# Kernel tuning notes

Measured on AMD Instinct MI355X. Metric: run time of the kernel, lower is better.

The kernel has to match this reference:

```python
import jax, jax.numpy as jnp
import numpy as np

NUM_HEADS = 8
KEY_DIM = 512      # total projected dim across heads
VALUE_DIM = 512
EMBED_DIM = 512


def setup_inputs() -> dict:
    key = jax.random.key(0)
    ks = jax.random.split(key, 12)
    B, S, E = 8, 1024, EMBED_DIM
    sc_in = 1.0 / np.sqrt(E)
    sc_o = 1.0 / np.sqrt(KEY_DIM)
    return {
        "queries": jax.random.normal(ks[0], (B, S, E), jnp.float32),
        "keys": jax.random.normal(ks[1], (B, S, E), jnp.float32),
        "values": jax.random.normal(ks[2], (B, S, E), jnp.float32),
        "Wq": jax.random.normal(ks[3], (E, KEY_DIM), jnp.float32) * sc_in,
        "bq": jnp.zeros((KEY_DIM,), jnp.float32),
        "Wk": jax.random.normal(ks[4], (E, KEY_DIM), jnp.float32) * sc_in,
        "bk": jnp.zeros((KEY_DIM,), jnp.float32),
        "Wv": jax.random.normal(ks[5], (E, VALUE_DIM), jnp.float32) * sc_in,
        "bv": jnp.zeros((VALUE_DIM,), jnp.float32),
        "Wo": jax.random.normal(ks[6], (KEY_DIM, EMBED_DIM), jnp.float32) * sc_o,
        "bo": jnp.zeros((EMBED_DIM,), jnp.float32),
    }


def _split_heads(x):
    # [B, S, key_dim] -> [B, H, S, key_dim//H]
    B, S, D = x.shape
    return x.reshape(B, S, NUM_HEADS, D // NUM_HEADS).transpose(0, 2, 1, 3)


def reference(queries, keys, values, Wq, bq, Wk, bk, Wv, bv, Wo, bo):
    q = _split_heads(queries @ Wq + bq)   # [B,H,S,dh]
    k = _split_heads(keys @ Wk + bk)
    v = _split_heads(values @ Wv + bv)
    # NOTE: original scales by sqrt(full key_dim), not per-head dim
    scores = jnp.einsum("bhqd,bhkd->bhqk", q, k) / jnp.sqrt(
        jnp.asarray(KEY_DIM, jnp.float32))
    weights = jax.nn.softmax(scores, axis=-1)
    o = jnp.einsum("bhqk,bhkd->bhqd", weights, v)  # [B,H,S,dh]
    B, H, S, dh = o.shape
    o = o.transpose(0, 2, 1, 3).reshape(B, S, H * dh)  # merge heads -> key_dim
    return o @ Wo + bo
```

## Files before the change

### kernel.cpp

```cpp
#include <hip/hip_runtime.h>


typedef __bf16 bf16x8 __attribute__((ext_vector_type(8)));
typedef __bf16 bf16x4 __attribute__((ext_vector_type(4)));
typedef float  f32x4  __attribute__((ext_vector_type(4)));

#define MFMA(a, b, c) __builtin_amdgcn_mfma_f32_16x16x32_bf16((a), (b), (c), 0, 0, 0)

__device__ inline bf16x8 cvt8(const float* p) {
  f32x4 u = *(const f32x4*)p;
  f32x4 v = *(const f32x4*)(p + 4);
  bf16x8 r;
  r[0] = (__bf16)u[0]; r[1] = (__bf16)u[1]; r[2] = (__bf16)u[2]; r[3] = (__bf16)u[3];
  r[4] = (__bf16)v[0]; r[5] = (__bf16)v[1]; r[6] = (__bf16)v[2]; r[7] = (__bf16)v[3];
  return r;
}

__device__ inline void gl_lds(const __bf16* g, __bf16* l) {
  __builtin_amdgcn_global_load_lds((const __attribute__((address_space(1))) void*)g,
                                   (__attribute__((address_space(3))) void*)l, 16, 0, 0);
}

__global__ __launch_bounds__(256) void cvt_qkv(const float* __restrict__ Q,
                                               const float* __restrict__ K,
                                               const float* __restrict__ V,
                                               __bf16* __restrict__ Qo,
                                               __bf16* __restrict__ Ko,
                                               __bf16* __restrict__ Vo) {
  const float* src;
  __bf16* dst;
  switch (blockIdx.y) {
    case 0: src = Q; dst = Qo; break;
    case 1: src = K; dst = Ko; break;
    default: src = V; dst = Vo; break;
  }
  const long idx = ((long)blockIdx.x * 256 + threadIdx.x) * 8;
  *(bf16x8*)(dst + idx) = cvt8(src + idx);
}

__global__ __launch_bounds__(256) void transpose_w4(const float* __restrict__ W0,
                                                    const float* __restrict__ W1,
                                                    const float* __restrict__ W2,
                                                    const float* __restrict__ W3,
                                                    __bf16* __restrict__ O0,
                                                    __bf16* __restrict__ O1,
                                                    __bf16* __restrict__ O2,
                                                    __bf16* __restrict__ O3,
                                                    float s0) {
  const float* in;
  __bf16* out;
  float sc = 1.0f;
  switch (blockIdx.y) {
    case 0: in = W0; out = O0; sc = s0; break;
    case 1: in = W1; out = O1; break;
    case 2: in = W2; out = O2; break;
    default: in = W3; out = O3; break;
  }
  __shared__ __align__(16) float t[64][65];
  const int tk = (blockIdx.x & 7) * 64;
  const int tn = (blockIdx.x >> 3) * 64;
  const int r0 = threadIdx.x >> 4;
  const int c4 = threadIdx.x & 15;
#pragma unroll
  for (int i = 0; i < 4; ++i) {
    int r = r0 + i * 16;
    f32x4 v = *(const f32x4*)(in + (long)(tk + r) * 512 + tn + c4 * 4);
#pragma unroll
    for (int j = 0; j < 4; ++j) t[r][c4 * 4 + j] = v[j] * sc;
  }
  __syncthreads();
  const int n0 = threadIdx.x >> 3;
  const int k8 = threadIdx.x & 7;
#pragma unroll
  for (int i = 0; i < 2; ++i) {
    int n = n0 + i * 32;
    bf16x8 v;
#pragma unroll
    for (int j = 0; j < 8; ++j) v[j] = (__bf16)t[k8 * 8 + j][n];
    *(bf16x8*)(out + (long)(tn + n) * 512 + tk + k8 * 8) = v;
  }
}

__global__ __launch_bounds__(256) void transpose_v(const __bf16* __restrict__ in,
                                                   __bf16* __restrict__ out) {
  __shared__ __align__(16) __bf16 t[64][72];
  const int pair = blockIdx.x >> 4;
  const int c = blockIdx.x & 15;
  const __bf16* ib = in + (long)pair * 65536 + c * 64 * 64;
  __bf16* ob = out + (long)pair * 65536 + c * 4096;
  const int r0 = threadIdx.x >> 3;
  const int c8 = threadIdx.x & 7;
#pragma unroll
  for (int i = 0; i < 2; ++i) {
    int s = r0 + i * 32;
    bf16x8 v = *(const bf16x8*)(ib + (long)s * 64 + c8 * 8);
#pragma unroll
    for (int j = 0; j < 8; ++j) t[s][c8 * 8 + j] = v[j];
  }
  __syncthreads();
#pragma unroll
  for (int i = 0; i < 2; ++i) {
    int d = r0 + i * 32;
    bf16x8 v;
#pragma unroll
    for (int j = 0; j < 8; ++j) v[j] = t[c8 * 8 + j][d];
    *(bf16x8*)(ob + d * 64 + ((c8 ^ (d & 7)) << 3)) = v;
  }
}

template <int MODE, typename OT>
__device__ __forceinline__ void gemm_core(const __bf16* __restrict__ X,
                                          const __bf16* __restrict__ Wt,
                                          const float* __restrict__ bias,
                                          OT* __restrict__ out, float bsc,
                                          __bf16 (*At)[4096], __bf16 (*Bt)[4096]) {
  const int tid = threadIdx.x;
  const int lane = tid & 63, wid = tid >> 6, quad = lane >> 4, l16 = lane & 15;
  const int i = blockIdx.x;
  const int kk = i >> 3;
  const int bm = ((i & 7) * 8 + (kk >> 2)) * 128;
  const int bn = (kk & 3) * 128;
  const int wm = (wid >> 1) * 64;
  const int wn = (wid & 1) * 64;

  const int rowInG = lane >> 2;
  const int blk = (lane & 3) ^ (rowInG & 3);
  const int ldsOff = lane * 8;

  f32x4 acc[4][4] = {};

#define STAGE(bi, k0)                                                          \
  {                                                                            \
    _Pragma("unroll") for (int j = 0; j < 2; ++j) {                            \
      const int g = wid * 2 + j;                                               \
      const int grow = g * 16 + rowInG;                                        \
      gl_lds(X + (long)(bm + grow) * 512 + (k0) + blk * 8,                     \
             &At[bi][g * 512 + ldsOff]);                                       \
      gl_lds(Wt + (long)(bn + grow) * 512 + (k0) + blk * 8,                    \
             &Bt[bi][g * 512 + ldsOff]);                                       \
    }                                                                          \
  }

  STAGE(0, 0);

  const int posm = quad ^ (l16 & 3);
  for (int c = 0; c < 16; ++c) {
    const int bi = c & 1;
    __syncthreads();
    if (c < 15) STAGE(bi ^ 1, (c + 1) * 32);

    bf16x8 a[4], b[4];
#pragma unroll
    for (int t = 0; t < 4; ++t) {
      a[t] = *(const bf16x8*)(&At[bi][(wm + t * 16 + l16) * 32 + (posm << 3)]);
      b[t] = *(const bf16x8*)(&Bt[bi][(wn + t * 16 + l16) * 32 + (posm << 3)]);
    }
#pragma unroll
    for (int mt = 0; mt < 4; ++mt)
#pragma unroll
      for (int nt = 0; nt < 4; ++nt) acc[mt][nt] = MFMA(a[mt], b[nt], acc[mt][nt]);
  }
#undef STAGE

#pragma unroll
  for (int nt = 0; nt < 4; ++nt) {
    const int n = bn + wn + nt * 16 + l16;
    const float bvv = bias[n] * bsc;
    const int h = n >> 6, d = n & 63;
#pragma unroll
    for (int mt = 0; mt < 4; ++mt) {
#pragma unroll
      for (int r = 0; r < 4; ++r) {
        const int m = bm + wm + mt * 16 + quad * 4 + r;
        const float v = acc[mt][nt][r] + bvv;
        if constexpr (MODE == 0) {
          out[(long)m * 512 + n] = (OT)v;
        } else if constexpr (MODE == 1) {
          const int bb = m >> 10, s = m & 1023;
          out[((long)((bb * 8 + h) * 1024 + s)) * 64 + d] = (OT)v;
        } else {
          const int bb = m >> 10, s = m & 1023;
          const long idx = (long)(bb * 8 + h) * 65536 + (s >> 6) * 4096 +
                           (s & 63) * 64 + (((d >> 3) ^ (s & 7)) << 3) + (d & 7);
          out[idx] = (OT)v;
        }
      }
    }
  }
}

__global__ __launch_bounds__(256) void gemm_qkv(
    const __bf16* __restrict__ Qx, const __bf16* __restrict__ Kx,
    const __bf16* __restrict__ Vx, const __bf16* __restrict__ Wqt,
    const __bf16* __restrict__ Wkt, const __bf16* __restrict__ Wvt,
    const float* __restrict__ bq, const float* __restrict__ bk,
    const float* __restrict__ bv, __bf16* __restrict__ Qp,
    __bf16* __restrict__ Kp, __bf16* __restrict__ Vp, float qscale) {
  __shared__ __align__(16) __bf16 At[2][4096];
  __shared__ __align__(16) __bf16 Bt[2][4096];
  if (blockIdx.y == 0)
    gemm_core<1, __bf16>(Qx, Wqt, bq, Qp, qscale, At, Bt);
  else if (blockIdx.y == 1)
    gemm_core<3, __bf16>(Kx, Wkt, bk, Kp, 1.0f, At, Bt);
  else
    gemm_core<1, __bf16>(Vx, Wvt, bv, Vp, 1.0f, At, Bt);
}

__global__ __launch_bounds__(256) void gemm_o(const __bf16* __restrict__ Oc,
                                              const __bf16* __restrict__ Wot,
                                              const float* __restrict__ bo,
                                              float* __restrict__ out) {
  __shared__ __align__(16) __bf16 At[2][4096];
  __shared__ __align__(16) __bf16 Bt[2][4096];
  gemm_core<0, float>(Oc, Wot, bo, out, 1.0f, At, Bt);
}

__global__ __launch_bounds__(256) void attn(const __bf16* __restrict__ Q,
                                            const __bf16* __restrict__ K,
                                            const __bf16* __restrict__ Vt,
                                            __bf16* __restrict__ Oc) {
  __shared__ __align__(16) __bf16 kbuf[2][4096];
  __shared__ __align__(16) __bf16 vbuf[2][4096];
  __shared__ __align__(16) __bf16 plds[4][32 * 64];

  const int tid = threadIdx.x;
  const int lane = tid & 63, wid = tid >> 6, quad = lane >> 4, l16 = lane & 15;
  const int i = blockIdx.x;
  const int pair = (i & 7) + (((i >> 6) & 7) << 3);
  const int qt = (i >> 3) & 7;
  const int q0 = qt * 128 + wid * 32;
  const int b = pair >> 3, h = pair & 7;
  const int swz = l16 & 7;

  const __bf16* Qb = Q + (long)pair * 65536;
  const __bf16* Kb = K + (long)pair * 65536;
  const __bf16* Vb = Vt + (long)pair * 65536;
  __bf16* pw = plds[wid];

  bf16x8 bq[2][2];
#pragma unroll
  for (int t = 0; t < 2; ++t)
#pragma unroll
    for (int e = 0; e < 2; ++e)
      bq[t][e] = *(const bf16x8*)(Qb + (q0 + t * 16 + l16) * 64 + e * 32 + quad * 8);

  float lr[2] = {0.f, 0.f};
  f32x4 oa[2][4] = {};

  {
    const __bf16* kg = Kb + tid * 8;
    const __bf16* vg = Vb + tid * 8;
    gl_lds(kg, &kbuf[0][tid * 8]);
    gl_lds(kg + 2048, &kbuf[0][2048 + tid * 8]);
    gl_lds(vg, &vbuf[0][tid * 8]);
    gl_lds(vg + 2048, &vbuf[0][2048 + tid * 8]);
  }

  for (int c = 0; c < 16; ++c) {
    const int bi = c & 1;
    __syncthreads();
    if (c < 15) {
      const __bf16* kg = Kb + (c + 1) * 4096 + tid * 8;
      const __bf16* vg = Vb + (c + 1) * 4096 + tid * 8;
      gl_lds(kg, &kbuf[bi ^ 1][tid * 8]);
      gl_lds(kg + 2048, &kbuf[bi ^ 1][2048 + tid * 8]);
      gl_lds(vg, &vbuf[bi ^ 1][tid * 8]);
      gl_lds(vg + 2048, &vbuf[bi ^ 1][2048 + tid * 8]);
    }

    f32x4 s[2][4] = {};
#pragma unroll
    for (int kt = 0; kt < 4; ++kt) {
      const int krow = (kt * 16 + l16) * 64;
      bf16x8 a0 = *(const bf16x8*)(&kbuf[bi][krow + ((quad ^ swz) << 3)]);
      bf16x8 a1 = *(const bf16x8*)(&kbuf[bi][krow + (((4 + quad) ^ swz) << 3)]);
#pragma unroll
      for (int t = 0; t < 2; ++t) {
        s[t][kt] = MFMA(a0, bq[t][0], s[t][kt]);
        s[t][kt] = MFMA(a1, bq[t][1], s[t][kt]);
      }
    }

#pragma unroll
    for (int t = 0; t < 2; ++t) {
      const int prow = (t * 16 + l16) * 64;
#pragma unroll
      for (int kt = 0; kt < 4; ++kt) {
        bf16x4 w;
#pragma unroll
        for (int r = 0; r < 4; ++r) {
          const float p = __expf(s[t][kt][r]);
          lr[t] += p;
          w[r] = (__bf16)p;
        }
        *(bf16x4*)(&pw[prow + (((kt * 2 + (quad >> 1)) ^ swz) << 3) + (quad & 1) * 4]) = w;
      }
    }
    bf16x8 pb[2][2];
#pragma unroll
    for (int t = 0; t < 2; ++t)
#pragma unroll
      for (int e = 0; e < 2; ++e)
        pb[t][e] = *(const bf16x8*)(&pw[(t * 16 + l16) * 64 + (((e * 4 + quad) ^ swz) << 3)]);

#pragma unroll
    for (int nt = 0; nt < 4; ++nt) {
      const int drow = (nt * 16 + l16) * 64;
      bf16x8 v0 = *(const bf16x8*)(&vbuf[bi][drow + ((quad ^ swz) << 3)]);
      bf16x8 v1 = *(const bf16x8*)(&vbuf[bi][drow + (((4 + quad) ^ swz) << 3)]);
#pragma unroll
      for (int t = 0; t < 2; ++t) {
        oa[t][nt] = MFMA(v0, pb[t][0], oa[t][nt]);
        oa[t][nt] = MFMA(v1, pb[t][1], oa[t][nt]);
      }
    }
  }

#pragma unroll
  for (int t = 0; t < 2; ++t) {
    lr[t] += __shfl_xor(lr[t], 16);
    lr[t] += __shfl_xor(lr[t], 32);
    const float inv = 1.0f / lr[t];
    const long base = ((long)b * 1024 + q0 + t * 16 + l16) * 512 + h * 64 + quad * 4;
#pragma unroll
    for (int nt = 0; nt < 4; ++nt) {
      bf16x4 w;
#pragma unroll
      for (int r = 0; r < 4; ++r) w[r] = (__bf16)(oa[t][nt][r] * inv);
      *(bf16x4*)(Oc + base + nt * 16) = w;
    }
  }
}

extern "C" void kernel_launch(void* const* d_in, const int* in_sizes, int n_in,
                              void* d_out, int out_size, void* d_ws, size_t ws_size,
                              hipStream_t stream) {
  const float* queries = (const float*)d_in[0];
  const float* keys = (const float*)d_in[1];
  const float* values = (const float*)d_in[2];
  const float* Wq = (const float*)d_in[3];
  const float* bq = (const float*)d_in[4];
  const float* Wk = (const float*)d_in[5];
  const float* bk = (const float*)d_in[6];
  const float* Wv = (const float*)d_in[7];
  const float* bv = (const float*)d_in[8];
  const float* Wo = (const float*)d_in[9];
  const float* bo = (const float*)d_in[10];
  float* out = (float*)d_out;

  __bf16* ws = (__bf16*)d_ws;
  const long WSZ = 512 * 512;
  const long XSZ = 8192L * 512;
  __bf16* Wqt = ws;
  __bf16* Wkt = ws + WSZ;
  __bf16* Wvt = ws + 2 * WSZ;
  __bf16* Wot = ws + 3 * WSZ;
  __bf16* Qp = ws + 4 * WSZ;
  __bf16* Kp = Qp + XSZ;
  __bf16* Vp = Kp + XSZ;
  __bf16* Vtp = Vp + XSZ;
  __bf16* Oc = Vtp + XSZ;
  __bf16* Qbf = Oc + XSZ;
  __bf16* Kbf = Qbf + XSZ;
  __bf16* Vbf = Kbf + XSZ;

  const float qscale = 0.04419417382415922f;

  cvt_qkv<<<dim3(2048, 3), 256, 0, stream>>>(queries, keys, values, Qbf, Kbf, Vbf);
  transpose_w4<<<dim3(64, 4), 256, 0, stream>>>(Wq, Wk, Wv, Wo, Wqt, Wkt, Wvt, Wot,
                                                qscale);

  gemm_qkv<<<dim3(256, 3), 256, 0, stream>>>(Qbf, Kbf, Vbf, Wqt, Wkt, Wvt, bq, bk, bv,
                                             Qp, Kp, Vp, qscale);

  transpose_v<<<1024, 256, 0, stream>>>(Vp, Vtp);

  attn<<<512, 256, 0, stream>>>(Qp, Kp, Vtp, Oc);

  gemm_o<<<256, 256, 0, stream>>>(Oc, Wot, bo, out);
}
```

Before: 181.9 us.

## Fuse fp32-to-bf16 input conversion and V transpose into QKV projection GEMM

Drops the separate cvt_qkv kernel: the QKV GEMM now streams fp32 activations straight into LDS with a swizzled layout and converts them to bf16 when loading MFMA fragments. The separate V transpose kernel is also removed, since the V projection epilogue now writes the transposed, swizzled layout for attention through an LDS staging buffer. This saves two kernel launches and a full read/write round trip of the bf16 activation and V buffers. In exchange, LDS per block grows to 48KB, fp32 tiles double the global-to-LDS traffic inside the GEMM, and the conversion now happens on the GEMM's inner loop.

```diff
diff --git a/kernel.cpp b/kernel.cpp
--- a/kernel.cpp
+++ b/kernel.cpp
@@ -7,35 +7,13 @@
 
 #define MFMA(a, b, c) __builtin_amdgcn_mfma_f32_16x16x32_bf16((a), (b), (c), 0, 0, 0)
 
-__device__ inline bf16x8 cvt8(const float* p) {
-  f32x4 u = *(const f32x4*)p;
-  f32x4 v = *(const f32x4*)(p + 4);
-  bf16x8 r;
-  r[0] = (__bf16)u[0]; r[1] = (__bf16)u[1]; r[2] = (__bf16)u[2]; r[3] = (__bf16)u[3];
-  r[4] = (__bf16)v[0]; r[5] = (__bf16)v[1]; r[6] = (__bf16)v[2]; r[7] = (__bf16)v[3];
-  return r;
-}
-
 __device__ inline void gl_lds(const __bf16* g, __bf16* l) {
   __builtin_amdgcn_global_load_lds((const __attribute__((address_space(1))) void*)g,
                                    (__attribute__((address_space(3))) void*)l, 16, 0, 0);
 }
-
-__global__ __launch_bounds__(256) void cvt_qkv(const float* __restrict__ Q,
-                                               const float* __restrict__ K,
-                                               const float* __restrict__ V,
-                                               __bf16* __restrict__ Qo,
-                                               __bf16* __restrict__ Ko,
-                                               __bf16* __restrict__ Vo) {
-  const float* src;
-  __bf16* dst;
-  switch (blockIdx.y) {
-    case 0: src = Q; dst = Qo; break;
-    case 1: src = K; dst = Ko; break;
-    default: src = V; dst = Vo; break;
-  }
-  const long idx = ((long)blockIdx.x * 256 + threadIdx.x) * 8;
-  *(bf16x8*)(dst + idx) = cvt8(src + idx);
+__device__ inline void gl_lds_f(const float* g, float* l) {
+  __builtin_amdgcn_global_load_lds((const __attribute__((address_space(1))) void*)g,
+                                   (__attribute__((address_space(3))) void*)l, 16, 0, 0);
 }
 
 __global__ __launch_bounds__(256) void transpose_w4(const float* __restrict__ W0,
@@ -81,39 +59,15 @@
   }
 }
 
-__global__ __launch_bounds__(256) void transpose_v(const __bf16* __restrict__ in,
-                                                   __bf16* __restrict__ out) {
-  __shared__ __align__(16) __bf16 t[64][72];
-  const int pair = blockIdx.x >> 4;
-  const int c = blockIdx.x & 15;
-  const __bf16* ib = in + (long)pair * 65536 + c * 64 * 64;
-  __bf16* ob = out + (long)pair * 65536 + c * 4096;
-  const int r0 = threadIdx.x >> 3;
-  const int c8 = threadIdx.x & 7;
-#pragma unroll
-  for (int i = 0; i < 2; ++i) {
-    int s = r0 + i * 32;
-    bf16x8 v = *(const bf16x8*)(ib + (long)s * 64 + c8 * 8);
-#pragma unroll
-    for (int j = 0; j < 8; ++j) t[s][c8 * 8 + j] = v[j];
-  }
-  __syncthreads();
-#pragma unroll
-  for (int i = 0; i < 2; ++i) {
-    int d = r0 + i * 32;
-    bf16x8 v;
-#pragma unroll
-    for (int j = 0; j < 8; ++j) v[j] = t[c8 * 8 + j][d];
-    *(bf16x8*)(ob + d * 64 + ((c8 ^ (d & 7)) << 3)) = v;
-  }
-}
-
-template <int MODE, typename OT>
-__device__ __forceinline__ void gemm_core(const __bf16* __restrict__ X,
+template <int MODE, typename XT, typename OT>
+__device__ __forceinline__ void gemm_core(const XT* __restrict__ X,
                                           const __bf16* __restrict__ Wt,
                                           const float* __restrict__ bias,
                                           OT* __restrict__ out, float bsc,
-                                          __bf16 (*At)[4096], __bf16 (*Bt)[4096]) {
+                                          char* smem) {
+  XT (*Af)[4096] = (XT(*)[4096])smem;
+  __bf16 (*Bt)[4096] = (__bf16(*)[4096])(smem + 2 * 4096 * sizeof(XT));
+
   const int tid = threadIdx.x;
   const int lane = tid & 63, wid = tid >> 6, quad = lane >> 4, l16 = lane & 15;
   const int i = blockIdx.x;
@@ -123,26 +77,39 @@
   const int wm = (wid >> 1) * 64;
   const int wn = (wid & 1) * 64;
 
-  const int rowInG = lane >> 2;
-  const int blk = (lane & 3) ^ (rowInG & 3);
-  const int ldsOff = lane * 8;
-
   f32x4 acc[4][4] = {};
+
+  const int rowB = lane >> 2;
+  const int gB = (lane & 3) ^ (rowB & 3);
+  const int rowA8 = lane >> 3;
+  const int gA = (lane & 7) ^ rowA8;
 
 #define STAGE(bi, k0)                                                          \
   {                                                                            \
+    if constexpr (__is_same(XT, float)) {                                      \
+      _Pragma("unroll") for (int j = 0; j < 4; ++j) {                          \
+        const int g = wid * 4 + j;                        \
+        gl_lds_f(X + (long)(bm + g * 8 + rowA8) * 512 + (k0) + (gA << 2),      \
+                 &Af[bi][g * 256 + lane * 4]);                                 \
+      }                                                                        \
+    } else {                                                                   \
+      _Pragma("unroll") for (int j = 0; j < 2; ++j) {                          \
+        const int g = wid * 2 + j;                     \
+        gl_lds((const __bf16*)X + (long)(bm + g * 16 + rowB) * 512 + (k0) +    \
+                   (gB << 3),                                                  \
+               (__bf16*)&Af[bi][g * 512 + lane * 8]);                          \
+      }                                                                        \
+    }                                                                          \
     _Pragma("unroll") for (int j = 0; j < 2; ++j) {                            \
       const int g = wid * 2 + j;                                               \
-      const int grow = g * 16 + rowInG;                                        \
-      gl_lds(X + (long)(bm + grow) * 512 + (k0) + blk * 8,                     \
-             &At[bi][g * 512 + ldsOff]);                                       \
-      gl_lds(Wt + (long)(bn + grow) * 512 + (k0) + blk * 8,                    \
-             &Bt[bi][g * 512 + ldsOff]);                                       \
+      gl_lds(Wt + (long)(bn + g * 16 + rowB) * 512 + (k0) + (gB << 3),         \
+             &Bt[bi][g * 512 + lane * 8]);                                     \
     }                                                                          \
   }
 
   STAGE(0, 0);
 
+  const int r7 = l16 & 7;
   const int posm = quad ^ (l16 & 3);
   for (int c = 0; c < 16; ++c) {
     const int bi = c & 1;
@@ -152,7 +119,20 @@
     bf16x8 a[4], b[4];
 #pragma unroll
     for (int t = 0; t < 4; ++t) {
-      a[t] = *(const bf16x8*)(&At[bi][(wm + t * 16 + l16) * 32 + (posm << 3)]);
+      if constexpr (__is_same(XT, float)) {
+        const float* rp = (const float*)&Af[bi][(wm + t * 16 + l16) * 32];
+        f32x4 u = *(const f32x4*)(rp + ((((quad << 1) | 0) ^ r7) << 2));
+        f32x4 v = *(const f32x4*)(rp + ((((quad << 1) | 1) ^ r7) << 2));
+        bf16x8 aa;
+        aa[0] = (__bf16)u[0]; aa[1] = (__bf16)u[1];
+        aa[2] = (__bf16)u[2]; aa[3] = (__bf16)u[3];
+        aa[4] = (__bf16)v[0]; aa[5] = (__bf16)v[1];
+        aa[6] = (__bf16)v[2]; aa[7] = (__bf16)v[3];
+        a[t] = aa;
+      } else {
+        a[t] = *(const bf16x8*)((const __bf16*)&Af[bi][0] +
+                                (wm + t * 16 + l16) * 32 + (posm << 3));
+      }
       b[t] = *(const bf16x8*)(&Bt[bi][(wn + t * 16 + l16) * 32 + (posm << 3)]);
     }
 #pragma unroll
@@ -161,6 +141,37 @@
       for (int nt = 0; nt < 4; ++nt) acc[mt][nt] = MFMA(a[mt], b[nt], acc[mt][nt]);
   }
 #undef STAGE
+
+  if constexpr (MODE == 4) {
+    __syncthreads();
+    __bf16* tb = (__bf16*)smem;
+#pragma unroll
+    for (int nt = 0; nt < 4; ++nt) {
+      const int n = wn + nt * 16 + l16;
+      const float bvv = bias[bn + n] * bsc;
+#pragma unroll
+      for (int mt = 0; mt < 4; ++mt) {
+        const int m0 = wm + mt * 16 + quad * 4;
+        bf16x4 w;
+#pragma unroll
+        for (int r = 0; r < 4; ++r) w[r] = (__bf16)(acc[mt][nt][r] + bvv);
+        *(bf16x4*)(&tb[n * 128 + (((m0 >> 3) ^ (n & 15)) << 3) + (m0 & 7)]) = w;
+      }
+    }
+    __syncthreads();
+    const int nn = tid & 127, mhalf = tid >> 7;
+    const int d = nn & 63, h = (bn + nn) >> 6;
+    const int bb = bm >> 10;
+    OT* ob = out + (long)(bb * 8 + h) * 65536;
+#pragma unroll
+    for (int gi = 0; gi < 8; ++gi) {
+      const int gl = mhalf * 8 + gi;
+      bf16x8 v = *(const bf16x8*)(&tb[nn * 128 + ((gl ^ (nn & 15)) << 3)]);
+      const int cidx = ((bm & 1023) + (gl << 3)) >> 6;
+      *(bf16x8*)(ob + cidx * 4096 + d * 64 + ((gi ^ (d & 7)) << 3)) = v;
+    }
+    return;
+  }
 
 #pragma unroll
   for (int nt = 0; nt < 4; ++nt) {
@@ -190,29 +201,27 @@
 }
 
 __global__ __launch_bounds__(256) void gemm_qkv(
-    const __bf16* __restrict__ Qx, const __bf16* __restrict__ Kx,
-    const __bf16* __restrict__ Vx, const __bf16* __restrict__ Wqt,
+    const float* __restrict__ Qx, const float* __restrict__ Kx,
+    const float* __restrict__ Vx, const __bf16* __restrict__ Wqt,
     const __bf16* __restrict__ Wkt, const __bf16* __restrict__ Wvt,
     const float* __restrict__ bq, const float* __restrict__ bk,
     const float* __restrict__ bv, __bf16* __restrict__ Qp,
-    __bf16* __restrict__ Kp, __bf16* __restrict__ Vp, float qscale) {
-  __shared__ __align__(16) __bf16 At[2][4096];
-  __shared__ __align__(16) __bf16 Bt[2][4096];
+    __bf16* __restrict__ Kp, __bf16* __restrict__ Vtp, float qscale) {
+  __shared__ __align__(16) char smem[49152];
   if (blockIdx.y == 0)
-    gemm_core<1, __bf16>(Qx, Wqt, bq, Qp, qscale, At, Bt);
+    gemm_core<1, float, __bf16>(Qx, Wqt, bq, Qp, qscale, smem);
   else if (blockIdx.y == 1)
-    gemm_core<3, __bf16>(Kx, Wkt, bk, Kp, 1.0f, At, Bt);
+    gemm_core<3, float, __bf16>(Kx, Wkt, bk, Kp, 1.0f, smem);
   else
-    gemm_core<1, __bf16>(Vx, Wvt, bv, Vp, 1.0f, At, Bt);
+    gemm_core<4, float, __bf16>(Vx, Wvt, bv, Vtp, 1.0f, smem);
 }
 
 __global__ __launch_bounds__(256) void gemm_o(const __bf16* __restrict__ Oc,
                                               const __bf16* __restrict__ Wot,
                                               const float* __restrict__ bo,
                                               float* __restrict__ out) {
-  __shared__ __align__(16) __bf16 At[2][4096];
-  __shared__ __align__(16) __bf16 Bt[2][4096];
-  gemm_core<0, float>(Oc, Wot, bo, out, 1.0f, At, Bt);
+  __shared__ __align__(16) char smem[32768];
+  gemm_core<0, __bf16, float>(Oc, Wot, bo, out, 1.0f, smem);
 }
 
 __global__ __launch_bounds__(256) void attn(const __bf16* __restrict__ Q,
@@ -357,23 +366,16 @@
   __bf16* Wot = ws + 3 * WSZ;
   __bf16* Qp = ws + 4 * WSZ;
   __bf16* Kp = Qp + XSZ;
-  __bf16* Vp = Kp + XSZ;
-  __bf16* Vtp = Vp + XSZ;
+  __bf16* Vtp = Kp + XSZ;
   __bf16* Oc = Vtp + XSZ;
-  __bf16* Qbf = Oc + XSZ;
-  __bf16* Kbf = Qbf + XSZ;
-  __bf16* Vbf = Kbf + XSZ;
 
   const float qscale = 0.04419417382415922f;
 
-  cvt_qkv<<<dim3(2048, 3), 256, 0, stream>>>(queries, keys, values, Qbf, Kbf, Vbf);
   transpose_w4<<<dim3(64, 4), 256, 0, stream>>>(Wq, Wk, Wv, Wo, Wqt, Wkt, Wvt, Wot,
                                                 qscale);
 
-  gemm_qkv<<<dim3(256, 3), 256, 0, stream>>>(Qbf, Kbf, Vbf, Wqt, Wkt, Wvt, bq, bk, bv,
-                                             Qp, Kp, Vp, qscale);
-
-  transpose_v<<<1024, 256, 0, stream>>>(Vp, Vtp);
+  gemm_qkv<<<dim3(256, 3), 256, 0, stream>>>(queries, keys, values, Wqt, Wkt, Wvt,
+                                             bq, bk, bv, Qp, Kp, Vtp, qscale);
 
   attn<<<512, 256, 0, stream>>>(Qp, Kp, Vtp, Oc);
 
```

After: 180.9 us. No clear change (-0.5%).

## Fuse V transpose into QKV GEMM epilogue via LDS-staged write

Applied to the files above, without the earlier changes.

Drops the separate transpose_v kernel. The V projection now uses a new epilogue mode that stages the bf16 tile in shared memory and writes it straight out in the transposed, swizzled layout that the attention kernel reads. This removes one kernel launch and a full read and write of the V intermediate. The LDS swizzle used for the A and B tiles also changes from a row-based to a row-pair-based XOR pattern. The cost is extra syncs and LDS traffic in the V blocks' epilogue.

```diff
diff --git a/kernel.cpp b/kernel.cpp
--- a/kernel.cpp
+++ b/kernel.cpp
@@ -81,39 +81,15 @@
   }
 }
 
-__global__ __launch_bounds__(256) void transpose_v(const __bf16* __restrict__ in,
-                                                   __bf16* __restrict__ out) {
-  __shared__ __align__(16) __bf16 t[64][72];
-  const int pair = blockIdx.x >> 4;
-  const int c = blockIdx.x & 15;
-  const __bf16* ib = in + (long)pair * 65536 + c * 64 * 64;
-  __bf16* ob = out + (long)pair * 65536 + c * 4096;
-  const int r0 = threadIdx.x >> 3;
-  const int c8 = threadIdx.x & 7;
-#pragma unroll
-  for (int i = 0; i < 2; ++i) {
-    int s = r0 + i * 32;
-    bf16x8 v = *(const bf16x8*)(ib + (long)s * 64 + c8 * 8);
-#pragma unroll
-    for (int j = 0; j < 8; ++j) t[s][c8 * 8 + j] = v[j];
-  }
-  __syncthreads();
-#pragma unroll
-  for (int i = 0; i < 2; ++i) {
-    int d = r0 + i * 32;
-    bf16x8 v;
-#pragma unroll
-    for (int j = 0; j < 8; ++j) v[j] = t[c8 * 8 + j][d];
-    *(bf16x8*)(ob + d * 64 + ((c8 ^ (d & 7)) << 3)) = v;
-  }
-}
-
 template <int MODE, typename OT>
 __device__ __forceinline__ void gemm_core(const __bf16* __restrict__ X,
                                           const __bf16* __restrict__ Wt,
                                           const float* __restrict__ bias,
                                           OT* __restrict__ out, float bsc,
-                                          __bf16 (*At)[4096], __bf16 (*Bt)[4096]) {
+                                          char* smem) {
+  __bf16 (*At)[4096] = (__bf16(*)[4096])smem;
+  __bf16 (*Bt)[4096] = (__bf16(*)[4096])(smem + 16384);
+
   const int tid = threadIdx.x;
   const int lane = tid & 63, wid = tid >> 6, quad = lane >> 4, l16 = lane & 15;
   const int i = blockIdx.x;
@@ -123,27 +99,25 @@
   const int wm = (wid >> 1) * 64;
   const int wn = (wid & 1) * 64;
 
-  const int rowInG = lane >> 2;
-  const int blk = (lane & 3) ^ (rowInG & 3);
-  const int ldsOff = lane * 8;
-
   f32x4 acc[4][4] = {};
+
+  const int rowB = lane >> 2;
+  const int gB = (lane & 3) ^ ((rowB >> 1) & 3);
 
 #define STAGE(bi, k0)                                                          \
   {                                                                            \
     _Pragma("unroll") for (int j = 0; j < 2; ++j) {                            \
-      const int g = wid * 2 + j;                                               \
-      const int grow = g * 16 + rowInG;                                        \
-      gl_lds(X + (long)(bm + grow) * 512 + (k0) + blk * 8,                     \
-             &At[bi][g * 512 + ldsOff]);                                       \
-      gl_lds(Wt + (long)(bn + grow) * 512 + (k0) + blk * 8,                    \
-             &Bt[bi][g * 512 + ldsOff]);                                       \
+      const int g = wid * 2 + j;                       \
+      gl_lds(X + (long)(bm + g * 16 + rowB) * 512 + (k0) + (gB << 3),          \
+             &At[bi][g * 512 + lane * 8]);                                     \
+      gl_lds(Wt + (long)(bn + g * 16 + rowB) * 512 + (k0) + (gB << 3),         \
+             &Bt[bi][g * 512 + lane * 8]);                                     \
     }                                                                          \
   }
 
   STAGE(0, 0);
 
-  const int posm = quad ^ (l16 & 3);
+  const int posm = quad ^ ((l16 >> 1) & 3);
   for (int c = 0; c < 16; ++c) {
     const int bi = c & 1;
     __syncthreads();
@@ -161,6 +135,37 @@
       for (int nt = 0; nt < 4; ++nt) acc[mt][nt] = MFMA(a[mt], b[nt], acc[mt][nt]);
   }
 #undef STAGE
+
+  if constexpr (MODE == 4) {
+    __syncthreads();
+    __bf16* tb = (__bf16*)smem;
+#pragma unroll
+    for (int nt = 0; nt < 4; ++nt) {
+      const int n = wn + nt * 16 + l16;
+      const float bvv = bias[bn + n] * bsc;
+#pragma unroll
+      for (int mt = 0; mt < 4; ++mt) {
+        const int m0 = wm + mt * 16 + quad * 4;
+        bf16x4 w;
+#pragma unroll
+        for (int r = 0; r < 4; ++r) w[r] = (__bf16)(acc[mt][nt][r] + bvv);
+        *(bf16x4*)(&tb[n * 128 + (((m0 >> 3) ^ (n & 15)) << 3) + (m0 & 7)]) = w;
+      }
+    }
+    __syncthreads();
+    const int nn = tid & 127, mhalf = tid >> 7;
+    const int d = nn & 63, h = (bn + nn) >> 6;
+    const int bb = bm >> 10;
+    OT* ob = out + (long)(bb * 8 + h) * 65536;
+#pragma unroll
+    for (int gi = 0; gi < 8; ++gi) {
+      const int gl = mhalf * 8 + gi;
+      bf16x8 v = *(const bf16x8*)(&tb[nn * 128 + ((gl ^ (nn & 15)) << 3)]);
+      const int cidx = ((bm & 1023) + (gl << 3)) >> 6;
+      *(bf16x8*)(ob + cidx * 4096 + d * 64 + ((gi ^ (d & 7)) << 3)) = v;
+    }
+    return;
+  }
 
 #pragma unroll
   for (int nt = 0; nt < 4; ++nt) {
@@ -195,24 +200,22 @@
     const __bf16* __restrict__ Wkt, const __bf16* __restrict__ Wvt,
     const float* __restrict__ bq, const float* __restrict__ bk,
     const float* __restrict__ bv, __bf16* __restrict__ Qp,
-    __bf16* __restrict__ Kp, __bf16* __restrict__ Vp, float qscale) {
-  __shared__ __align__(16) __bf16 At[2][4096];
-  __shared__ __align__(16) __bf16 Bt[2][4096];
+    __bf16* __restrict__ Kp, __bf16* __restrict__ Vtp, float qscale) {
+  __shared__ __align__(16) char smem[32768];
   if (blockIdx.y == 0)
-    gemm_core<1, __bf16>(Qx, Wqt, bq, Qp, qscale, At, Bt);
+    gemm_core<1, __bf16>(Qx, Wqt, bq, Qp, qscale, smem);
   else if (blockIdx.y == 1)
-    gemm_core<3, __bf16>(Kx, Wkt, bk, Kp, 1.0f, At, Bt);
+    gemm_core<3, __bf16>(Kx, Wkt, bk, Kp, 1.0f, smem);
   else
-    gemm_core<1, __bf16>(Vx, Wvt, bv, Vp, 1.0f, At, Bt);
+    gemm_core<4, __bf16>(Vx, Wvt, bv, Vtp, 1.0f, smem);
 }
 
 __global__ __launch_bounds__(256) void gemm_o(const __bf16* __restrict__ Oc,
                                               const __bf16* __restrict__ Wot,
                                               const float* __restrict__ bo,
                                               float* __restrict__ out) {
-  __shared__ __align__(16) __bf16 At[2][4096];
-  __shared__ __align__(16) __bf16 Bt[2][4096];
-  gemm_core<0, float>(Oc, Wot, bo, out, 1.0f, At, Bt);
+  __shared__ __align__(16) char smem[32768];
+  gemm_core<0, float>(Oc, Wot, bo, out, 1.0f, smem);
 }
 
 __global__ __launch_bounds__(256) void attn(const __bf16* __restrict__ Q,
@@ -357,8 +360,7 @@
   __bf16* Wot = ws + 3 * WSZ;
   __bf16* Qp = ws + 4 * WSZ;
   __bf16* Kp = Qp + XSZ;
-  __bf16* Vp = Kp + XSZ;
-  __bf16* Vtp = Vp + XSZ;
+  __bf16* Vtp = Kp + XSZ;
   __bf16* Oc = Vtp + XSZ;
   __bf16* Qbf = Oc + XSZ;
   __bf16* Kbf = Qbf + XSZ;
@@ -370,10 +372,8 @@
   transpose_w4<<<dim3(64, 4), 256, 0, stream>>>(Wq, Wk, Wv, Wo, Wqt, Wkt, Wvt, Wot,
                                                 qscale);
 
-  gemm_qkv<<<dim3(256, 3), 256, 0, stream>>>(Qbf, Kbf, Vbf, Wqt, Wkt, Wvt, bq, bk, bv,
-                                             Qp, Kp, Vp, qscale);
-
-  transpose_v<<<1024, 256, 0, stream>>>(Vp, Vtp);
+  gemm_qkv<<<dim3(256, 3), 256, 0, stream>>>(Qbf, Kbf, Vbf, Wqt, Wkt, Wvt,
+                                             bq, bk, bv, Qp, Kp, Vtp, qscale);
 
   attn<<<512, 256, 0, stream>>>(Qp, Kp, Vtp, Oc);
 
```

After: 174.8 us. -3.9%, faster.
